# Kernel optimization log

Measured on AMD Instinct MI355X. Metric: run time of the kernel, lower is better.

The kernel has to match this reference:

```python
import jax, jax.numpy as jnp
import numpy as np
from jax import lax

B, C, H, W = 32, 684, 16, 64
HID, A, CK, K = 256, 512, 512, 11


def setup_inputs() -> dict:
    key = jax.random.key(0)
    ks = jax.random.split(key, 12)
    s = 0.02
    return {
        "cnn_features": jax.random.normal(ks[0], (B, C, H, W), jnp.float32),
        "hidden": jax.random.normal(ks[1], (B, HID), jnp.float32),
        "alpha_sum": jax.random.uniform(ks[2], (B, 1, H, W), jnp.float32),
        "image_mask": jnp.ones((B, 1, H, W), jnp.float32),
        # hidden_weight: Linear(HID -> A)
        "Wh": jax.random.normal(ks[3], (A, HID), jnp.float32) * s,
        "bh": jnp.zeros((A,), jnp.float32),
        # encoder_feature_conv: Conv2d(C -> A, 1x1) == pointwise linear
        "Wec": jax.random.normal(ks[4], (A, C), jnp.float32) * s,
        "bec": jnp.zeros((A,), jnp.float32),
        # attention_conv: Conv2d(1 -> CK, 11x11, pad 5, no bias)
        "Wac": jax.random.normal(ks[5], (CK, 1, K, K), jnp.float32) * s,
        # attention_weight: Linear(CK -> A, no bias)
        "Waw": jax.random.normal(ks[6], (A, CK), jnp.float32) * s,
        # alpha_convert: Linear(A -> 1)
        "Wv": jax.random.normal(ks[7], (1, A), jnp.float32) * s,
        "bv": jnp.zeros((1,), jnp.float32),
    }


def reference(cnn_features, hidden, alpha_sum, image_mask,
              Wh, bh, Wec, bec, Wac, Waw, Wv, bv):
    # query = hidden_weight(hidden): [B, A]
    query = hidden @ Wh.T + bh
    # attention_conv(alpha_sum): [B, CK, H, W]
    ast = lax.conv_general_dilated(
        alpha_sum, Wac, window_strides=(1, 1),
        padding=[(K // 2, K // 2), (K // 2, K // 2)],
        dimension_numbers=("NCHW", "OIHW", "NCHW"))
    # attention_weight on permuted conv output: [B, H, W, A]
    coverage_alpha = jnp.einsum("bkhw,ak->bhwa", ast, Waw)
    # encoder_feature_conv (1x1 conv == pointwise linear): [B, H, W, A]
    cnn_trans = jnp.einsum("bchw,ac->bhwa", cnn_features, Wec) + bec
    # additive attention score
    alpha_score = jnp.tanh(query[:, None, None, :] + coverage_alpha + cnn_trans)
    # alpha_convert -> scalar energy per position: [B, H, W]
    energy = jnp.einsum("bhwa,a->bhw", alpha_score, Wv[0]) + bv[0]
    energy = energy - energy.max()  # global max-subtract as in original
    energy_exp = jnp.exp(energy) * image_mask[:, 0]
    denom = energy_exp.sum(axis=(-1, -2))[:, None, None] + 1e-10
    alpha = energy_exp / denom  # [B, H, W]
    alpha_sum_new = alpha[:, None, :, :] + alpha_sum  # [B, 1, H, W]
    # context: weighted spatial sum over features -> [B, C]
    context_vector = jnp.einsum("bhw,bchw->bc", alpha, cnn_features)
    return (context_vector, alpha, alpha_sum_new)
```

## Files before the change

kernel.cpp:

```cpp
#include <hip/hip_runtime.h>
#include <math.h>

#define Bn   32
#define Cn   684
#define Hn   16
#define Wn   64
#define HWn  1024
#define HIDn 256
#define An   512
#define KKn  121
#define CREAL 805
#define CPAD 832
#define NSTEP 26
#define NBLK 256

#define OUT_ALPHA 21888
#define OUT_ASUM  (21888 + 32768)

typedef short short8 __attribute__((ext_vector_type(8)));
typedef float floatx4 __attribute__((ext_vector_type(4)));

__device__ __forceinline__ unsigned short f2bf(float f) {
    union { float f; unsigned int i; } v; v.f = f;
    unsigned int i = v.i;
    return (unsigned short)((i + 0x7fffu + ((i >> 16) & 1u)) >> 16);
}
__device__ __forceinline__ unsigned int pack2bf(float v0, float v1) {
    unsigned int u0 = __float_as_uint(v0), u1 = __float_as_uint(v1);
    u0 = (u0 + 0x7fffu + ((u0 >> 16) & 1u)) >> 16;
    u1 = (u1 + 0x7fffu + ((u1 >> 16) & 1u)) & 0xffff0000u;
    return u0 | u1;
}

__global__ __launch_bounds__(256) void k_prep(
    const float* __restrict__ hidden,
    const float* __restrict__ Wh,
    const float* __restrict__ bh,
    const float* __restrict__ bec,
    const float* __restrict__ Wec,
    const float* __restrict__ Wac,
    const float* __restrict__ Waw,
    float* __restrict__ query,
    unsigned short* __restrict__ VTbf)
{
    __shared__ float sbuf[512];
    __shared__ float wac_s[64 * KKn];
    const int blk = blockIdx.x, t = threadIdx.x;
    if (blk < 512) {
        const int a = blk;
        sbuf[t]       = Waw[(size_t)a * 512 + t];
        sbuf[t + 256] = Waw[(size_t)a * 512 + t + 256];
        for (int cp = t; cp < Cn; cp += 256)
            VTbf[(size_t)a * CPAD + cp] = f2bf(Wec[(size_t)a * Cn + cp]);
        float s = 0.f;
        for (int kb = 0; kb < 8; ++kb) {
            __syncthreads();
            for (int i = t; i < 64 * KKn; i += 256)
                wac_s[i] = Wac[kb * 64 * KKn + i];
            __syncthreads();
            if (t < KKn) {
                #pragma unroll 8
                for (int kk = 0; kk < 64; ++kk)
                    s = fmaf(sbuf[kb * 64 + kk], wac_s[kk * KKn + t], s);
            }
        }
        if (t < KKn)
            VTbf[(size_t)a * CPAD + Cn + t] = f2bf(s);
        for (int cp = CREAL + t; cp < CPAD; cp += 256)
            VTbf[(size_t)a * CPAD + cp] = 0;
    } else {
        const int b = blk - 512;
        sbuf[t] = (t < HIDn) ? hidden[b * HIDn + t] : 0.f;
        __syncthreads();
        for (int a = t; a < An; a += 256) {
            const float4* wp = (const float4*)(Wh + (size_t)a * HIDn);
            float s = bh[a] + bec[a];
            #pragma unroll 8
            for (int i = 0; i < HIDn / 4; ++i) {
                float4 w = wp[i];
                s = fmaf(sbuf[4 * i],     w.x, s);
                s = fmaf(sbuf[4 * i + 1], w.y, s);
                s = fmaf(sbuf[4 * i + 2], w.z, s);
                s = fmaf(sbuf[4 * i + 3], w.w, s);
            }
            query[b * An + a] = s;
        }
    }
}

__device__ __forceinline__ float fetchU(const float* __restrict__ Xb,
                                        const float* plane,
                                        int m, int row) {
    if (row < Cn)   return Xb[(size_t)row * HWn + m];
    if (row < CREAL) {
        int ij = row - Cn; int di = ij / 11, dj = ij - di * 11;
        return plane[di * 74 + m + dj];
    }
    return 0.f;
}

__global__ __launch_bounds__(256, 4) void k_energy(
    const float* __restrict__ X,
    const float* __restrict__ asum,
    const float* __restrict__ Wv,
    const float* __restrict__ query,
    const unsigned short* __restrict__ VTbf,
    float* __restrict__ energy)
{
    __shared__ unsigned short As[2 * 64 * 40];
    __shared__ float red[64 * 65];
    __shared__ float plane[11 * 74 + 2];
    __shared__ float qs[NBLK];
    __shared__ float wvs[NBLK];

    const int t = threadIdx.x;
    const int nh = blockIdx.x, hh = blockIdx.y, b = blockIdx.z;
    const int w = t >> 6, lane = t & 63;
    const int q = lane >> 4, r = lane & 15;
    const int nbase = nh * NBLK;
    const int mA = t & 63;
    const int koA = t >> 6;

    const float* Xb = X + (size_t)b * Cn * HWn + hh * Wn;
    const unsigned short* Bw = VTbf + (size_t)(nbase + w * 64) * CPAD;

    for (int i = t; i < 11 * 74; i += 256) {
        int di = i / 74, cc = i - di * 74;
        int h2 = hh + di - 5, w2 = cc - 5;
        float v = 0.f;
        if (h2 >= 0 && h2 < Hn && w2 >= 0 && w2 < Wn)
            v = asum[b * HWn + h2 * Wn + w2];
        plane[i] = v;
    }
    qs[t]  = query[b * An + nbase + t];
    wvs[t] = Wv[nbase + t];

    {
        const float* xp = Xb + (size_t)(koA * 8) * HWn + mA;
        unsigned int pk[4];
        #pragma unroll
        for (int jj = 0; jj < 4; ++jj)
            pk[jj] = pack2bf(xp[(size_t)(2 * jj) * HWn], xp[(size_t)(2 * jj + 1) * HWn]);
        *(uint4*)&As[mA * 40 + koA * 8] = make_uint4(pk[0], pk[1], pk[2], pk[3]);
    }
    float xpref[8];
    {
        const float* xp = Xb + (size_t)(32 + koA * 8) * HWn + mA;
        #pragma unroll
        for (int jj = 0; jj < 8; ++jj) xpref[jj] = xp[(size_t)jj * HWn];
    }
    short8 bfr[4];
    #pragma unroll
    for (int nf = 0; nf < 4; ++nf)
        bfr[nf] = *(const short8*)(Bw + (size_t)(nf * 16 + r) * CPAD + q * 8);
    __syncthreads();

    floatx4 acc[4][4];
    #pragma unroll
    for (int mf = 0; mf < 4; ++mf)
        #pragma unroll
        for (int nf = 0; nf < 4; ++nf)
            acc[mf][nf] = (floatx4){0.f, 0.f, 0.f, 0.f};

    for (int ch = 0; ch < NSTEP; ++ch) {
        const int cur = ch & 1;
        short8 af[4];
        #pragma unroll
        for (int mf = 0; mf < 4; ++mf)
            af[mf] = *(const short8*)&As[cur * (64 * 40) + (mf * 16 + r) * 40 + q * 8];
        #pragma unroll
        for (int mf = 0; mf < 4; ++mf)
            #pragma unroll
            for (int nf = 0; nf < 4; ++nf)
                acc[mf][nf] = __builtin_amdgcn_mfma_f32_16x16x32_bf16(
                    af[mf], bfr[nf], acc[mf][nf], 0, 0, 0);
        if (ch + 1 < NSTEP) {
            const int c1 = (ch + 1) * 32;
            #pragma unroll
            for (int nf = 0; nf < 4; ++nf)
                bfr[nf] = *(const short8*)(Bw + (size_t)(nf * 16 + r) * CPAD + c1 + q * 8);
            unsigned int pk[4];
            #pragma unroll
            for (int jj = 0; jj < 4; ++jj)
                pk[jj] = pack2bf(xpref[2 * jj], xpref[2 * jj + 1]);
            *(uint4*)&As[(cur ^ 1) * (64 * 40) + mA * 40 + koA * 8] =
                make_uint4(pk[0], pk[1], pk[2], pk[3]);
        }
        if (ch + 2 < NSTEP) {
            const int c2 = (ch + 2) * 32;
            if (c2 + 31 < Cn) {
                const float* xp = Xb + (size_t)(c2 + koA * 8) * HWn + mA;
                #pragma unroll
                for (int jj = 0; jj < 8; ++jj) xpref[jj] = xp[(size_t)jj * HWn];
            } else {
                #pragma unroll
                for (int jj = 0; jj < 8; ++jj)
                    xpref[jj] = fetchU(Xb, plane, mA, c2 + koA * 8 + jj);
            }
        }
        __syncthreads();
    }

    float ep[16];
    #pragma unroll
    for (int i = 0; i < 16; ++i) ep[i] = 0.f;
    #pragma unroll
    for (int nf = 0; nf < 4; ++nf) {
        int nl = w * 64 + nf * 16 + r;
        float qv = qs[nl], wv = wvs[nl];
        #pragma unroll
        for (int mf = 0; mf < 4; ++mf)
            #pragma unroll
            for (int rg = 0; rg < 4; ++rg) {
                float x = acc[mf][nf][rg] + qv;
                float e2 = __expf(2.f * x);
                float th = 1.f - 2.f * __builtin_amdgcn_rcpf(e2 + 1.f);
                ep[mf * 4 + rg] += wv * th;
            }
    }
    #pragma unroll
    for (int mf = 0; mf < 4; ++mf)
        #pragma unroll
        for (int rg = 0; rg < 4; ++rg)
            red[(mf * 16 + q * 4 + rg) * 65 + w * 16 + r] = ep[mf * 4 + rg];
    __syncthreads();
    if (t < 64) {
        float s = 0.f;
        #pragma unroll 16
        for (int i = 0; i < 64; ++i) s += red[t * 65 + i];
        energy[(size_t)nh * (Bn * HWn) + b * HWn + hh * Wn + t] = s;
    }
}

__global__ __launch_bounds__(256) void k_ctx(
    const float* __restrict__ X,
    const float* __restrict__ energy,
    const float* __restrict__ mask,
    const float* __restrict__ asum,
    float* __restrict__ out)
{
    __shared__ float al[1024];
    __shared__ float rsm[8];
    const int bx = blockIdx.x, b = blockIdx.y;
    const int t = threadIdx.x, lane = t & 63, wid = t >> 6;

    float e[4], ex[4];
    #pragma unroll
    for (int i = 0; i < 4; ++i) {
        int p = b * HWn + i * 256 + t;
        e[i] = energy[p] + energy[Bn * HWn + p];
    }
    float m = fmaxf(fmaxf(e[0], e[1]), fmaxf(e[2], e[3]));
    for (int off = 32; off >= 1; off >>= 1) m = fmaxf(m, __shfl_down(m, off, 64));
    if (lane == 0) rsm[wid] = m;
    __syncthreads();
    if (t == 0)
        rsm[4] = fmaxf(fmaxf(rsm[0], rsm[1]), fmaxf(rsm[2], rsm[3]));
    __syncthreads();
    const float M = rsm[4];
    float s = 0.f;
    #pragma unroll
    for (int i = 0; i < 4; ++i) {
        ex[i] = expf(e[i] - M) * mask[b * HWn + i * 256 + t];
        s += ex[i];
    }
    for (int off = 32; off >= 1; off >>= 1) s += __shfl_down(s, off, 64);
    __syncthreads();
    if (lane == 0) rsm[wid] = s;
    __syncthreads();
    if (t == 0) rsm[5] = rsm[0] + rsm[1] + rsm[2] + rsm[3] + 1e-10f;
    __syncthreads();
    const float denom = rsm[5];
    #pragma unroll
    for (int i = 0; i < 4; ++i) al[i * 256 + t] = ex[i] / denom;
    __syncthreads();

    const int c = bx * 4 + wid;
    const float* xp = X + ((size_t)(b * Cn + c)) * HWn;
    float s2 = 0.f;
    #pragma unroll
    for (int i = 0; i < 4; ++i) {
        int off = i * 256 + lane * 4;
        float4 x = *(const float4*)(xp + off);
        float4 a = *(const float4*)(al + off);
        s2 = fmaf(a.x, x.x, s2);
        s2 = fmaf(a.y, x.y, s2);
        s2 = fmaf(a.z, x.z, s2);
        s2 = fmaf(a.w, x.w, s2);
    }
    for (int off = 32; off >= 1; off >>= 1) s2 += __shfl_down(s2, off, 64);
    if (lane == 0) out[b * Cn + c] = s2;

    if (bx == 0) {
        #pragma unroll
        for (int i = 0; i < 4; ++i) {
            int p = i * 256 + t;
            float a = al[p];
            out[OUT_ALPHA + b * HWn + p] = a;
            out[OUT_ASUM  + b * HWn + p] = a + asum[b * HWn + p];
        }
    }
}

extern "C" void kernel_launch(void* const* d_in, const int* in_sizes, int n_in,
                              void* d_out, int out_size, void* d_ws, size_t ws_size,
                              hipStream_t stream)
{
    const float* X      = (const float*)d_in[0];
    const float* hidden = (const float*)d_in[1];
    const float* asum   = (const float*)d_in[2];
    const float* mask   = (const float*)d_in[3];
    const float* Wh     = (const float*)d_in[4];
    const float* bh     = (const float*)d_in[5];
    const float* Wec    = (const float*)d_in[6];
    const float* bec    = (const float*)d_in[7];
    const float* Wac    = (const float*)d_in[8];
    const float* Waw    = (const float*)d_in[9];
    const float* Wv     = (const float*)d_in[10];
    (void)in_sizes; (void)n_in; (void)out_size; (void)ws_size;

    float* out = (float*)d_out;
    float* ws = (float*)d_ws;
    float* query  = ws;
    float* energy = ws + 16384;
    unsigned short* VTbf = (unsigned short*)(ws + 16384 + 65536);

    k_prep   <<<dim3(544),       dim3(256), 0, stream>>>(hidden, Wh, bh, bec,
                                                         Wec, Wac, Waw, query, VTbf);
    k_energy <<<dim3(2, 16, 32), dim3(256), 0, stream>>>(X, asum, Wv, query, VTbf, energy);
    k_ctx    <<<dim3(171, 32),   dim3(256), 0, stream>>>(X, energy, mask, asum, out);
}
```

Baseline: 259.6 us.

## Pre-transpose features to bf16 and compute full-width energy GEMM per block

```diff
diff --git a/kernel.cpp b/kernel.cpp
--- a/kernel.cpp
+++ b/kernel.cpp
@@ -12,7 +12,6 @@
 #define CREAL 805
 #define CPAD 832
 #define NSTEP 26
-#define NBLK 256
 
 #define OUT_ALPHA 21888
 #define OUT_ASUM  (21888 + 32768)
@@ -20,6 +19,9 @@
 typedef short short8 __attribute__((ext_vector_type(8)));
 typedef float floatx4 __attribute__((ext_vector_type(4)));
 
+__device__ __forceinline__ float bf2f(unsigned short u) {
+    union { unsigned int i; float f; } v; v.i = ((unsigned int)u) << 16; return v.f;
+}
 __device__ __forceinline__ unsigned short f2bf(float f) {
     union { float f; unsigned int i; } v; v.f = f;
     unsigned int i = v.i;
@@ -33,6 +35,8 @@
 }
 
 __global__ __launch_bounds__(256) void k_prep(
+    const float* __restrict__ X,
+    const float* __restrict__ asum,
     const float* __restrict__ hidden,
     const float* __restrict__ Wh,
     const float* __restrict__ bh,
@@ -41,13 +45,55 @@
     const float* __restrict__ Wac,
     const float* __restrict__ Waw,
     float* __restrict__ query,
-    unsigned short* __restrict__ VTbf)
+    unsigned short* __restrict__ VTbf,
+    unsigned short* __restrict__ Xt)
 {
     __shared__ float sbuf[512];
     __shared__ float wac_s[64 * KKn];
+    __shared__ float plane[11 * 74 + 2];
     const int blk = blockIdx.x, t = threadIdx.x;
+
     if (blk < 512) {
-        const int a = blk;
+        const int b = blk >> 4, h = blk & 15;
+        for (int i = t; i < 11 * 74; i += 256) {
+            int di = i / 74, cc = i - di * 74;
+            int h2 = h + di - 5, w2 = cc - 5;
+            float v = 0.f;
+            if (h2 >= 0 && h2 < Hn && w2 >= 0 && w2 < Wn)
+                v = asum[b * HWn + h2 * Wn + w2];
+            plane[i] = v;
+        }
+        __syncthreads();
+        const int m = t >> 2, cq = t & 3;
+        const float* Xbh = X + (size_t)b * Cn * HWn + h * Wn;
+        unsigned short* Xr = Xt + (size_t)(b * HWn + h * Wn + m) * CPAD;
+        for (int cb = 0; cb < NSTEP; ++cb) {
+            const int c0 = cb * 32 + cq * 8;
+            float v[8];
+            if (c0 + 7 < Cn) {
+                #pragma unroll
+                for (int j = 0; j < 8; ++j)
+                    v[j] = Xbh[(size_t)(c0 + j) * HWn + m];
+            } else {
+                #pragma unroll
+                for (int j = 0; j < 8; ++j) {
+                    int c = c0 + j;
+                    float x;
+                    if (c < Cn) x = Xbh[(size_t)c * HWn + m];
+                    else if (c < CREAL) {
+                        int ij = c - Cn; int di = ij / 11, dj = ij - di * 11;
+                        x = plane[di * 74 + m + dj];
+                    } else x = 0.f;
+                    v[j] = x;
+                }
+            }
+            unsigned int pk[4];
+            #pragma unroll
+            for (int j = 0; j < 4; ++j) pk[j] = pack2bf(v[2 * j], v[2 * j + 1]);
+            *(uint4*)(Xr + c0) = make_uint4(pk[0], pk[1], pk[2], pk[3]);
+        }
+    } else if (blk < 1024) {
+        const int a = blk - 512;
         sbuf[t]       = Waw[(size_t)a * 512 + t];
         sbuf[t + 256] = Waw[(size_t)a * 512 + t + 256];
         for (int cp = t; cp < Cn; cp += 256)
@@ -69,7 +115,7 @@
         for (int cp = CREAL + t; cp < CPAD; cp += 256)
             VTbf[(size_t)a * CPAD + cp] = 0;
     } else {
-        const int b = blk - 512;
+        const int b = blk - 1024;
         sbuf[t] = (t < HIDn) ? hidden[b * HIDn + t] : 0.f;
         __syncthreads();
         for (int a = t; a < An; a += 256) {
@@ -88,126 +134,79 @@
     }
 }
 
-__device__ __forceinline__ float fetchU(const float* __restrict__ Xb,
-                                        const float* plane,
-                                        int m, int row) {
-    if (row < Cn)   return Xb[(size_t)row * HWn + m];
-    if (row < CREAL) {
-        int ij = row - Cn; int di = ij / 11, dj = ij - di * 11;
-        return plane[di * 74 + m + dj];
-    }
-    return 0.f;
-}
-
-__global__ __launch_bounds__(256, 4) void k_energy(
-    const float* __restrict__ X,
-    const float* __restrict__ asum,
+__global__ __launch_bounds__(256, 2) void k_energy(
+    const unsigned short* __restrict__ Xt,
     const float* __restrict__ Wv,
     const float* __restrict__ query,
     const unsigned short* __restrict__ VTbf,
     float* __restrict__ energy)
 {
-    __shared__ unsigned short As[2 * 64 * 40];
     __shared__ float red[64 * 65];
-    __shared__ float plane[11 * 74 + 2];
-    __shared__ float qs[NBLK];
-    __shared__ float wvs[NBLK];
+    __shared__ float qs[An];
+    __shared__ float wvs[An];
 
     const int t = threadIdx.x;
-    const int nh = blockIdx.x, hh = blockIdx.y, b = blockIdx.z;
+    const int hh = blockIdx.x, b = blockIdx.y;
     const int w = t >> 6, lane = t & 63;
     const int q = lane >> 4, r = lane & 15;
-    const int nbase = nh * NBLK;
-    const int mA = t & 63;
-    const int koA = t >> 6;
-
-    const float* Xb = X + (size_t)b * Cn * HWn + hh * Wn;
-    const unsigned short* Bw = VTbf + (size_t)(nbase + w * 64) * CPAD;
-
-    for (int i = t; i < 11 * 74; i += 256) {
-        int di = i / 74, cc = i - di * 74;
-        int h2 = hh + di - 5, w2 = cc - 5;
-        float v = 0.f;
-        if (h2 >= 0 && h2 < Hn && w2 >= 0 && w2 < Wn)
-            v = asum[b * HWn + h2 * Wn + w2];
-        plane[i] = v;
-    }
-    qs[t]  = query[b * An + nbase + t];
-    wvs[t] = Wv[nbase + t];
-
-    {
-        const float* xp = Xb + (size_t)(koA * 8) * HWn + mA;
-        unsigned int pk[4];
-        #pragma unroll
-        for (int jj = 0; jj < 4; ++jj)
-            pk[jj] = pack2bf(xp[(size_t)(2 * jj) * HWn], xp[(size_t)(2 * jj + 1) * HWn]);
-        *(uint4*)&As[mA * 40 + koA * 8] = make_uint4(pk[0], pk[1], pk[2], pk[3]);
-    }
-    float xpref[8];
-    {
-        const float* xp = Xb + (size_t)(32 + koA * 8) * HWn + mA;
-        #pragma unroll
-        for (int jj = 0; jj < 8; ++jj) xpref[jj] = xp[(size_t)jj * HWn];
-    }
-    short8 bfr[4];
-    #pragma unroll
-    for (int nf = 0; nf < 4; ++nf)
-        bfr[nf] = *(const short8*)(Bw + (size_t)(nf * 16 + r) * CPAD + q * 8);
-    __syncthreads();
-
-    floatx4 acc[4][4];
+
+    qs[t]        = query[b * An + t];
+    qs[t + 256]  = query[b * An + t + 256];
+    wvs[t]       = Wv[t];
+    wvs[t + 256] = Wv[t + 256];
+
+    const unsigned short* Arow = Xt + (size_t)(b * HWn + hh * Wn) * CPAD + r * CPAD + q * 8;
+    const unsigned short* Brow = VTbf + (size_t)(w * 128) * CPAD + r * CPAD + q * 8;
+
+    floatx4 acc[4][8];
     #pragma unroll
     for (int mf = 0; mf < 4; ++mf)
         #pragma unroll
-        for (int nf = 0; nf < 4; ++nf)
+        for (int nf = 0; nf < 8; ++nf)
             acc[mf][nf] = (floatx4){0.f, 0.f, 0.f, 0.f};
 
-    for (int ch = 0; ch < NSTEP; ++ch) {
-        const int cur = ch & 1;
-        short8 af[4];
-        #pragma unroll
-        for (int mf = 0; mf < 4; ++mf)
-            af[mf] = *(const short8*)&As[cur * (64 * 40) + (mf * 16 + r) * 40 + q * 8];
-        #pragma unroll
-        for (int mf = 0; mf < 4; ++mf)
-            #pragma unroll
-            for (int nf = 0; nf < 4; ++nf)
+    short8 af[4], bfA[8], bfB[8];
+    #pragma unroll
+    for (int nf = 0; nf < 8; ++nf)
+        bfA[nf] = *(const short8*)(Brow + (size_t)(nf * 16) * CPAD);
+
+    for (int ch = 0; ch < NSTEP; ch += 2) {
+        const int c0 = ch * 32;
+        #pragma unroll
+        for (int mf = 0; mf < 4; ++mf)
+            af[mf] = *(const short8*)(Arow + (size_t)(mf * 16) * CPAD + c0);
+        #pragma unroll
+        for (int nf = 0; nf < 8; ++nf)
+            bfB[nf] = *(const short8*)(Brow + (size_t)(nf * 16) * CPAD + c0 + 32);
+        #pragma unroll
+        for (int mf = 0; mf < 4; ++mf)
+            #pragma unroll
+            for (int nf = 0; nf < 8; ++nf)
                 acc[mf][nf] = __builtin_amdgcn_mfma_f32_16x16x32_bf16(
-                    af[mf], bfr[nf], acc[mf][nf], 0, 0, 0);
-        if (ch + 1 < NSTEP) {
-            const int c1 = (ch + 1) * 32;
-            #pragma unroll
-            for (int nf = 0; nf < 4; ++nf)
-                bfr[nf] = *(const short8*)(Bw + (size_t)(nf * 16 + r) * CPAD + c1 + q * 8);
-            unsigned int pk[4];
-            #pragma unroll
-            for (int jj = 0; jj < 4; ++jj)
-                pk[jj] = pack2bf(xpref[2 * jj], xpref[2 * jj + 1]);
-            *(uint4*)&As[(cur ^ 1) * (64 * 40) + mA * 40 + koA * 8] =
-                make_uint4(pk[0], pk[1], pk[2], pk[3]);
-        }
+                    af[mf], bfA[nf], acc[mf][nf], 0, 0, 0);
+        #pragma unroll
+        for (int mf = 0; mf < 4; ++mf)
+            af[mf] = *(const short8*)(Arow + (size_t)(mf * 16) * CPAD + c0 + 32);
         if (ch + 2 < NSTEP) {
-            const int c2 = (ch + 2) * 32;
-            if (c2 + 31 < Cn) {
-                const float* xp = Xb + (size_t)(c2 + koA * 8) * HWn + mA;
-                #pragma unroll
-                for (int jj = 0; jj < 8; ++jj) xpref[jj] = xp[(size_t)jj * HWn];
-            } else {
-                #pragma unroll
-                for (int jj = 0; jj < 8; ++jj)
-                    xpref[jj] = fetchU(Xb, plane, mA, c2 + koA * 8 + jj);
-            }
-        }
-        __syncthreads();
+            #pragma unroll
+            for (int nf = 0; nf < 8; ++nf)
+                bfA[nf] = *(const short8*)(Brow + (size_t)(nf * 16) * CPAD + c0 + 64);
+        }
+        #pragma unroll
+        for (int mf = 0; mf < 4; ++mf)
+            #pragma unroll
+            for (int nf = 0; nf < 8; ++nf)
+                acc[mf][nf] = __builtin_amdgcn_mfma_f32_16x16x32_bf16(
+                    af[mf], bfB[nf], acc[mf][nf], 0, 0, 0);
     }
 
     float ep[16];
     #pragma unroll
     for (int i = 0; i < 16; ++i) ep[i] = 0.f;
     #pragma unroll
-    for (int nf = 0; nf < 4; ++nf) {
-        int nl = w * 64 + nf * 16 + r;
-        float qv = qs[nl], wv = wvs[nl];
+    for (int nf = 0; nf < 8; ++nf) {
+        int n = w * 128 + nf * 16 + r;
+        float qv = qs[n], wv = wvs[n];
         #pragma unroll
         for (int mf = 0; mf < 4; ++mf)
             #pragma unroll
@@ -218,6 +217,7 @@
                 ep[mf * 4 + rg] += wv * th;
             }
     }
+    __syncthreads();
     #pragma unroll
     for (int mf = 0; mf < 4; ++mf)
         #pragma unroll
@@ -228,12 +228,12 @@
         float s = 0.f;
         #pragma unroll 16
         for (int i = 0; i < 64; ++i) s += red[t * 65 + i];
-        energy[(size_t)nh * (Bn * HWn) + b * HWn + hh * Wn + t] = s;
+        energy[b * HWn + hh * Wn + t] = s;
     }
 }
 
 __global__ __launch_bounds__(256) void k_ctx(
-    const float* __restrict__ X,
+    const unsigned short* __restrict__ Xt,
     const float* __restrict__ energy,
     const float* __restrict__ mask,
     const float* __restrict__ asum,
@@ -241,21 +241,17 @@
 {
     __shared__ float al[1024];
     __shared__ float rsm[8];
-    const int bx = blockIdx.x, b = blockIdx.y;
+    const int hhc = blockIdx.x, b = blockIdx.y;
     const int t = threadIdx.x, lane = t & 63, wid = t >> 6;
 
     float e[4], ex[4];
     #pragma unroll
-    for (int i = 0; i < 4; ++i) {
-        int p = b * HWn + i * 256 + t;
-        e[i] = energy[p] + energy[Bn * HWn + p];
-    }
+    for (int i = 0; i < 4; ++i) e[i] = energy[b * HWn + i * 256 + t];
     float m = fmaxf(fmaxf(e[0], e[1]), fmaxf(e[2], e[3]));
     for (int off = 32; off >= 1; off >>= 1) m = fmaxf(m, __shfl_down(m, off, 64));
     if (lane == 0) rsm[wid] = m;
     __syncthreads();
-    if (t == 0)
-        rsm[4] = fmaxf(fmaxf(rsm[0], rsm[1]), fmaxf(rsm[2], rsm[3]));
+    if (t == 0) rsm[4] = fmaxf(fmaxf(rsm[0], rsm[1]), fmaxf(rsm[2], rsm[3]));
     __syncthreads();
     const float M = rsm[4];
     float s = 0.f;
@@ -275,23 +271,30 @@
     for (int i = 0; i < 4; ++i) al[i * 256 + t] = ex[i] / denom;
     __syncthreads();
 
-    const int c = bx * 4 + wid;
-    const float* xp = X + ((size_t)(b * Cn + c)) * HWn;
-    float s2 = 0.f;
-    #pragma unroll
-    for (int i = 0; i < 4; ++i) {
-        int off = i * 256 + lane * 4;
-        float4 x = *(const float4*)(xp + off);
-        float4 a = *(const float4*)(al + off);
-        s2 = fmaf(a.x, x.x, s2);
-        s2 = fmaf(a.y, x.y, s2);
-        s2 = fmaf(a.z, x.z, s2);
-        s2 = fmaf(a.w, x.w, s2);
-    }
-    for (int off = 32; off >= 1; off >>= 1) s2 += __shfl_down(s2, off, 64);
-    if (lane == 0) out[b * Cn + c] = s2;
-
-    if (bx == 0) {
+    float c0a = 0.f, c0b = 0.f, c1a = 0.f, c1b = 0.f;
+    const int d0 = t, d1 = t + 256;
+    const unsigned int* Xr =
+        (const unsigned int*)(Xt + (size_t)(b * HWn + hhc * 64) * CPAD);
+    for (int hl = 0; hl < 64; ++hl) {
+        const float a = al[hhc * 64 + hl];
+        const unsigned int* row = Xr + (size_t)hl * (CPAD / 2);
+        unsigned int u0 = row[d0];
+        c0a = fmaf(a, bf2f((unsigned short)(u0 & 0xffffu)), c0a);
+        c0b = fmaf(a, bf2f((unsigned short)(u0 >> 16)),     c0b);
+        if (d1 < 342) {
+            unsigned int u1 = row[d1];
+            c1a = fmaf(a, bf2f((unsigned short)(u1 & 0xffffu)), c1a);
+            c1b = fmaf(a, bf2f((unsigned short)(u1 >> 16)),     c1b);
+        }
+    }
+    atomicAdd(&out[b * Cn + 2 * d0],     c0a);
+    atomicAdd(&out[b * Cn + 2 * d0 + 1], c0b);
+    if (d1 < 342) {
+        atomicAdd(&out[b * Cn + 2 * d1],     c1a);
+        atomicAdd(&out[b * Cn + 2 * d1 + 1], c1b);
+    }
+
+    if (hhc == 0) {
         #pragma unroll
         for (int i = 0; i < 4; ++i) {
             int p = i * 256 + t;
@@ -320,13 +323,14 @@
     (void)in_sizes; (void)n_in; (void)out_size; (void)ws_size;
 
     float* out = (float*)d_out;
-    float* ws = (float*)d_ws;
-    float* query  = ws;
-    float* energy = ws + 16384;
-    unsigned short* VTbf = (unsigned short*)(ws + 16384 + 65536);
-
-    k_prep   <<<dim3(544),       dim3(256), 0, stream>>>(hidden, Wh, bh, bec,
-                                                         Wec, Wac, Waw, query, VTbf);
-    k_energy <<<dim3(2, 16, 32), dim3(256), 0, stream>>>(X, asum, Wv, query, VTbf, energy);
-    k_ctx    <<<dim3(171, 32),   dim3(256), 0, stream>>>(X, energy, mask, asum, out);
-}
+    unsigned short* Xt   = (unsigned short*)d_ws;
+    unsigned short* VTbf = Xt + (size_t)Bn * HWn * CPAD;
+    float* query  = (float*)(VTbf + (size_t)An * CPAD);
+    float* energy = query + 16384;
+
+    hipMemsetAsync(out, 0, OUT_ALPHA * sizeof(float), stream);
+    k_prep   <<<dim3(1056),   dim3(256), 0, stream>>>(X, asum, hidden, Wh, bh, bec,
+                                                      Wec, Wac, Waw, query, VTbf, Xt);
+    k_energy <<<dim3(16, 32), dim3(256), 0, stream>>>(Xt, Wv, query, VTbf, energy);
+    k_ctx    <<<dim3(16, 32), dim3(256), 0, stream>>>(Xt, energy, mask, asum, out);
+}
```

Result: slower. 297.4 us (+14.6%).

## Cover all attention columns per energy block to halve feature re-reads

Applied to the files above, without the earlier changes.

```diff
diff --git a/kernel.cpp b/kernel.cpp
--- a/kernel.cpp
+++ b/kernel.cpp
@@ -12,7 +12,6 @@
 #define CREAL 805
 #define CPAD 832
 #define NSTEP 26
-#define NBLK 256
 
 #define OUT_ALPHA 21888
 #define OUT_ASUM  (21888 + 32768)
@@ -99,7 +98,7 @@
     return 0.f;
 }
 
-__global__ __launch_bounds__(256, 4) void k_energy(
+__global__ __launch_bounds__(256, 2) void k_energy(
     const float* __restrict__ X,
     const float* __restrict__ asum,
     const float* __restrict__ Wv,
@@ -110,19 +109,17 @@
     __shared__ unsigned short As[2 * 64 * 40];
     __shared__ float red[64 * 65];
     __shared__ float plane[11 * 74 + 2];
-    __shared__ float qs[NBLK];
-    __shared__ float wvs[NBLK];
+    __shared__ float qs[An];
+    __shared__ float wvs[An];
 
     const int t = threadIdx.x;
-    const int nh = blockIdx.x, hh = blockIdx.y, b = blockIdx.z;
+    const int hh = blockIdx.x, b = blockIdx.y;
     const int w = t >> 6, lane = t & 63;
     const int q = lane >> 4, r = lane & 15;
-    const int nbase = nh * NBLK;
-    const int mA = t & 63;
-    const int koA = t >> 6;
+    const int mA = lane, koA = w;
 
     const float* Xb = X + (size_t)b * Cn * HWn + hh * Wn;
-    const unsigned short* Bw = VTbf + (size_t)(nbase + w * 64) * CPAD;
+    const unsigned short* Brow = VTbf + (size_t)(w * 128 + r) * CPAD + q * 8;
 
     for (int i = t; i < 11 * 74; i += 256) {
         int di = i / 74, cc = i - di * 74;
@@ -132,8 +129,10 @@
             v = asum[b * HWn + h2 * Wn + w2];
         plane[i] = v;
     }
-    qs[t]  = query[b * An + nbase + t];
-    wvs[t] = Wv[nbase + t];
+    qs[t]        = query[b * An + t];
+    qs[t + 256]  = query[b * An + t + 256];
+    wvs[t]       = Wv[t];
+    wvs[t + 256] = Wv[t + 256];
 
     {
         const float* xp = Xb + (size_t)(koA * 8) * HWn + mA;
@@ -143,61 +142,97 @@
             pk[jj] = pack2bf(xp[(size_t)(2 * jj) * HWn], xp[(size_t)(2 * jj + 1) * HWn]);
         *(uint4*)&As[mA * 40 + koA * 8] = make_uint4(pk[0], pk[1], pk[2], pk[3]);
     }
-    float xpref[8];
+    float xpA[8], xpB[8];
     {
         const float* xp = Xb + (size_t)(32 + koA * 8) * HWn + mA;
         #pragma unroll
-        for (int jj = 0; jj < 8; ++jj) xpref[jj] = xp[(size_t)jj * HWn];
-    }
-    short8 bfr[4];
-    #pragma unroll
-    for (int nf = 0; nf < 4; ++nf)
-        bfr[nf] = *(const short8*)(Bw + (size_t)(nf * 16 + r) * CPAD + q * 8);
-    __syncthreads();
-
-    floatx4 acc[4][4];
+        for (int jj = 0; jj < 8; ++jj) xpA[jj] = xp[(size_t)jj * HWn];
+    }
+    {
+        const float* xp = Xb + (size_t)(64 + koA * 8) * HWn + mA;
+        #pragma unroll
+        for (int jj = 0; jj < 8; ++jj) xpB[jj] = xp[(size_t)jj * HWn];
+    }
+    short8 bfrA[8], bfrB[8], af[4];
+    #pragma unroll
+    for (int nf = 0; nf < 8; ++nf)
+        bfrA[nf] = *(const short8*)(Brow + (size_t)(nf * 16) * CPAD);
+    __syncthreads();
+
+    floatx4 acc[4][8];
     #pragma unroll
     for (int mf = 0; mf < 4; ++mf)
         #pragma unroll
-        for (int nf = 0; nf < 4; ++nf)
+        for (int nf = 0; nf < 8; ++nf)
             acc[mf][nf] = (floatx4){0.f, 0.f, 0.f, 0.f};
 
-    for (int ch = 0; ch < NSTEP; ++ch) {
-        const int cur = ch & 1;
-        short8 af[4];
-        #pragma unroll
-        for (int mf = 0; mf < 4; ++mf)
-            af[mf] = *(const short8*)&As[cur * (64 * 40) + (mf * 16 + r) * 40 + q * 8];
-        #pragma unroll
-        for (int mf = 0; mf < 4; ++mf)
-            #pragma unroll
-            for (int nf = 0; nf < 4; ++nf)
+    for (int i = 0; i < 13; ++i) {
+        const int ch0 = 2 * i, ch1 = 2 * i + 1;
+        #pragma unroll
+        for (int mf = 0; mf < 4; ++mf)
+            af[mf] = *(const short8*)&As[(mf * 16 + r) * 40 + q * 8];
+        #pragma unroll
+        for (int nf = 0; nf < 8; ++nf)
+            bfrB[nf] = *(const short8*)(Brow + (size_t)(nf * 16) * CPAD + ch1 * 32);
+        {
+            unsigned int pk[4];
+            #pragma unroll
+            for (int jj = 0; jj < 4; ++jj)
+                pk[jj] = pack2bf(xpA[2 * jj], xpA[2 * jj + 1]);
+            *(uint4*)&As[64 * 40 + mA * 40 + koA * 8] = make_uint4(pk[0], pk[1], pk[2], pk[3]);
+        }
+        if (2 * i + 3 < NSTEP) {
+            const int c3 = (2 * i + 3) * 32;
+            if (c3 + 31 < Cn) {
+                const float* xp = Xb + (size_t)(c3 + koA * 8) * HWn + mA;
+                #pragma unroll
+                for (int jj = 0; jj < 8; ++jj) xpA[jj] = xp[(size_t)jj * HWn];
+            } else {
+                #pragma unroll
+                for (int jj = 0; jj < 8; ++jj)
+                    xpA[jj] = fetchU(Xb, plane, mA, c3 + koA * 8 + jj);
+            }
+        }
+        #pragma unroll
+        for (int mf = 0; mf < 4; ++mf)
+            #pragma unroll
+            for (int nf = 0; nf < 8; ++nf)
                 acc[mf][nf] = __builtin_amdgcn_mfma_f32_16x16x32_bf16(
-                    af[mf], bfr[nf], acc[mf][nf], 0, 0, 0);
-        if (ch + 1 < NSTEP) {
-            const int c1 = (ch + 1) * 32;
-            #pragma unroll
-            for (int nf = 0; nf < 4; ++nf)
-                bfr[nf] = *(const short8*)(Bw + (size_t)(nf * 16 + r) * CPAD + c1 + q * 8);
-            unsigned int pk[4];
-            #pragma unroll
-            for (int jj = 0; jj < 4; ++jj)
-                pk[jj] = pack2bf(xpref[2 * jj], xpref[2 * jj + 1]);
-            *(uint4*)&As[(cur ^ 1) * (64 * 40) + mA * 40 + koA * 8] =
-                make_uint4(pk[0], pk[1], pk[2], pk[3]);
-        }
-        if (ch + 2 < NSTEP) {
-            const int c2 = (ch + 2) * 32;
-            if (c2 + 31 < Cn) {
-                const float* xp = Xb + (size_t)(c2 + koA * 8) * HWn + mA;
-                #pragma unroll
-                for (int jj = 0; jj < 8; ++jj) xpref[jj] = xp[(size_t)jj * HWn];
+                    af[mf], bfrA[nf], acc[mf][nf], 0, 0, 0);
+        __syncthreads();
+        #pragma unroll
+        for (int mf = 0; mf < 4; ++mf)
+            af[mf] = *(const short8*)&As[64 * 40 + (mf * 16 + r) * 40 + q * 8];
+        if (ch1 + 1 < NSTEP) {
+            #pragma unroll
+            for (int nf = 0; nf < 8; ++nf)
+                bfrA[nf] = *(const short8*)(Brow + (size_t)(nf * 16) * CPAD + (ch1 + 1) * 32);
+            {
+                unsigned int pk[4];
+                #pragma unroll
+                for (int jj = 0; jj < 4; ++jj)
+                    pk[jj] = pack2bf(xpB[2 * jj], xpB[2 * jj + 1]);
+                *(uint4*)&As[mA * 40 + koA * 8] = make_uint4(pk[0], pk[1], pk[2], pk[3]);
+            }
+        }
+        if (2 * i + 4 < NSTEP) {
+            const int c4 = (2 * i + 4) * 32;
+            if (c4 + 31 < Cn) {
+                const float* xp = Xb + (size_t)(c4 + koA * 8) * HWn + mA;
+                #pragma unroll
+                for (int jj = 0; jj < 8; ++jj) xpB[jj] = xp[(size_t)jj * HWn];
             } else {
                 #pragma unroll
                 for (int jj = 0; jj < 8; ++jj)
-                    xpref[jj] = fetchU(Xb, plane, mA, c2 + koA * 8 + jj);
-            }
-        }
+                    xpB[jj] = fetchU(Xb, plane, mA, c4 + koA * 8 + jj);
+            }
+        }
+        #pragma unroll
+        for (int mf = 0; mf < 4; ++mf)
+            #pragma unroll
+            for (int nf = 0; nf < 8; ++nf)
+                acc[mf][nf] = __builtin_amdgcn_mfma_f32_16x16x32_bf16(
+                    af[mf], bfrB[nf], acc[mf][nf], 0, 0, 0);
         __syncthreads();
     }
 
@@ -205,9 +240,9 @@
     #pragma unroll
     for (int i = 0; i < 16; ++i) ep[i] = 0.f;
     #pragma unroll
-    for (int nf = 0; nf < 4; ++nf) {
-        int nl = w * 64 + nf * 16 + r;
-        float qv = qs[nl], wv = wvs[nl];
+    for (int nf = 0; nf < 8; ++nf) {
+        int n = w * 128 + nf * 16 + r;
+        float qv = qs[n], wv = wvs[n];
         #pragma unroll
         for (int mf = 0; mf < 4; ++mf)
             #pragma unroll
@@ -228,7 +263,7 @@
         float s = 0.f;
         #pragma unroll 16
         for (int i = 0; i < 64; ++i) s += red[t * 65 + i];
-        energy[(size_t)nh * (Bn * HWn) + b * HWn + hh * Wn + t] = s;
+        energy[b * HWn + hh * Wn + t] = s;
     }
 }
 
@@ -246,16 +281,12 @@
 
     float e[4], ex[4];
     #pragma unroll
-    for (int i = 0; i < 4; ++i) {
-        int p = b * HWn + i * 256 + t;
-        e[i] = energy[p] + energy[Bn * HWn + p];
-    }
+    for (int i = 0; i < 4; ++i) e[i] = energy[b * HWn + i * 256 + t];
     float m = fmaxf(fmaxf(e[0], e[1]), fmaxf(e[2], e[3]));
     for (int off = 32; off >= 1; off >>= 1) m = fmaxf(m, __shfl_down(m, off, 64));
     if (lane == 0) rsm[wid] = m;
     __syncthreads();
-    if (t == 0)
-        rsm[4] = fmaxf(fmaxf(rsm[0], rsm[1]), fmaxf(rsm[2], rsm[3]));
+    if (t == 0) rsm[4] = fmaxf(fmaxf(rsm[0], rsm[1]), fmaxf(rsm[2], rsm[3]));
     __syncthreads();
     const float M = rsm[4];
     float s = 0.f;
@@ -323,10 +354,10 @@
     float* ws = (float*)d_ws;
     float* query  = ws;
     float* energy = ws + 16384;
-    unsigned short* VTbf = (unsigned short*)(ws + 16384 + 65536);
-
-    k_prep   <<<dim3(544),       dim3(256), 0, stream>>>(hidden, Wh, bh, bec,
-                                                         Wec, Wac, Waw, query, VTbf);
-    k_energy <<<dim3(2, 16, 32), dim3(256), 0, stream>>>(X, asum, Wv, query, VTbf, energy);
-    k_ctx    <<<dim3(171, 32),   dim3(256), 0, stream>>>(X, energy, mask, asum, out);
-}
+    unsigned short* VTbf = (unsigned short*)(ws + 16384 + 32768);
+
+    k_prep   <<<dim3(544),     dim3(256), 0, stream>>>(hidden, Wh, bh, bec,
+                                                       Wec, Wac, Waw, query, VTbf);
+    k_energy <<<dim3(16, 32),  dim3(256), 0, stream>>>(X, asum, Wv, query, VTbf, energy);
+    k_ctx    <<<dim3(171, 32), dim3(256), 0, stream>>>(X, energy, mask, asum, out);
+}
```

New measurement: 263.4 us. No clear change (+1.5%).
